# Kernel optimization log

Measured on AMD Instinct MI355X. Metric: run time of the kernel, lower is better.

The kernel has to match this reference:

```python
import jax, jax.numpy as jnp
import numpy as np

B, C, S, F = 128, 5, 512, 3
U = 256          # encoder units
RU = 2 * U       # decoder units / bidirectional encoder width


def _lstm_cell(x_t, h, c, Wk, Wr, b):
    # Keras LSTM gate order: i, f, g(cell), o
    z = x_t @ Wk + h @ Wr + b
    i, f, g, o = jnp.split(z, 4, axis=-1)
    c_new = jax.nn.sigmoid(f) * c + jax.nn.sigmoid(i) * jnp.tanh(g)
    h_new = jax.nn.sigmoid(o) * jnp.tanh(c_new)
    return h_new, c_new


def _masked_lstm(xs, mask, Wk, Wr, b, units):
    # xs: [B,S,D], mask: [B,S] bool. Keras semantics: masked steps carry
    # previous state and previous output (== previous h for LSTM).
    Bn = xs.shape[0]

    def step(carry, inp):
        h, c = carry
        x_t, m_t = inp
        h_n, c_n = _lstm_cell(x_t, h, c, Wk, Wr, b)
        m = m_t[:, None]
        h2 = jnp.where(m, h_n, h)
        c2 = jnp.where(m, c_n, c)
        return (h2, c2), h2

    init = (jnp.zeros((Bn, units), xs.dtype), jnp.zeros((Bn, units), xs.dtype))
    _, outs = jax.lax.scan(step, init, (jnp.swapaxes(xs, 0, 1), mask.T))
    return jnp.swapaxes(outs, 0, 1)  # [B,S,units]


def setup_inputs() -> dict:
    key = jax.random.key(0)
    k = jax.random.split(key, 10)
    s = 0.05
    rn = lambda kk, sh: jax.random.normal(kk, sh, jnp.float32) * s
    return {
        "x": jax.random.normal(k[0], (B, C, S, F), jnp.float32),
        "Wf_k": rn(k[1], (C, 4 * U)), "Wf_r": rn(k[2], (U, 4 * U)), "bf": jnp.zeros((4 * U,), jnp.float32),
        "Wb_k": rn(k[3], (C, 4 * U)), "Wb_r": rn(k[4], (U, 4 * U)), "bb": jnp.zeros((4 * U,), jnp.float32),
        "Wd_k": rn(k[5], (C, 4 * RU)), "Wd_r": rn(k[6], (RU, 4 * RU)), "bd": jnp.zeros((4 * RU,), jnp.float32),
        "W_attn": rn(k[7], (RU + C, 1)), "b_attn": jnp.zeros((1,), jnp.float32),
        "W_dense": rn(k[8], (RU + RU, C)), "b_dense": jnp.zeros((C,), jnp.float32),
    }


def reference(x, Wf_k, Wf_r, bf, Wb_k, Wb_r, bb, Wd_k, Wd_r, bd,
              W_attn, b_attn, W_dense, b_dense):
    xt = jnp.transpose(x, (0, 2, 1, 3))          # [B,S,C,F]
    mask = xt[:, :, 0, 2] != 0                   # tf.cast(..., bool)
    xs = xt[:, :, :, 0]                          # [B,S,C]

    fwd = _masked_lstm(xs, mask, Wf_k, Wf_r, bf, U)
    bwd = _masked_lstm(xs[:, ::-1], mask[:, ::-1], Wb_k, Wb_r, bb, U)[:, ::-1]
    enc = jnp.concatenate([fwd, bwd], axis=-1)   # [B,S,RU]

    # attention(concat([tile(x_t), enc])) is linear -> split the weight:
    Wx, We = W_attn[:C, 0], W_attn[C:, 0]
    enc_scores = jnp.einsum('bsd,d->bs', enc, We) + b_attn[0]  # [B,S]

    hidden0 = enc[:, -1, :]                      # [B,RU]
    x0 = xs[:, 0, :]                             # [B,C]

    def dec_step(carry, _):
        hidden, x_t = carry
        scores = enc_scores + (x_t @ Wx)[:, None]             # [B,S]
        alpha = jax.nn.softmax(scores, axis=1)
        attn = jnp.einsum('bs,bsd->bd', alpha, enc)           # [B,RU]
        # decoder LSTM on a single timestep, initial_state=[hidden, attn]
        h_new, _c = _lstm_cell(x_t, hidden, attn, Wd_k, Wd_r, bd)
        x_new = jnp.concatenate([h_new, attn], axis=-1) @ W_dense + b_dense
        return (h_new, x_new), x_new

    _, ys = jax.lax.scan(dec_step, (hidden0, x0), None, length=S - 1)  # [S-1,B,C]
    return jnp.transpose(ys, (1, 2, 0))[..., None]           # [B,C,S-1,1]
```

## Files before the change

kernel.cpp:

```cpp
#include <hip/hip_runtime.h>
#include <math.h>

#define BATCH 128
#define CCH 5
#define SEQ 512
#define UNITS 256
#define RU 512

#define ENC_N 33554432

__device__ __forceinline__ float sigmoidf_(float v) {
    return 1.0f / (1.0f + __expf(-v));
}
__device__ __forceinline__ float tanhf_(float v) {
    float e = __expf(2.0f * v);
    return 1.0f - 2.0f / (e + 1.0f);
}
__device__ __forceinline__ void astoref(float* p, float v) {
    __hip_atomic_store(p, v, __ATOMIC_RELAXED, __HIP_MEMORY_SCOPE_AGENT);
}
__device__ __forceinline__ void astorei(int* p, int v) {
    __hip_atomic_store(p, v, __ATOMIC_RELAXED, __HIP_MEMORY_SCOPE_AGENT);
}
__device__ __forceinline__ unsigned long long aloadu64(const unsigned long long* p) {
    return __hip_atomic_load(p, __ATOMIC_RELAXED, __HIP_MEMORY_SCOPE_AGENT);
}
__device__ __forceinline__ int aloadi(const int* p) {
    return __hip_atomic_load(p, __ATOMIC_RELAXED, __HIP_MEMORY_SCOPE_AGENT);
}

__global__ __attribute__((amdgpu_flat_work_group_size(1024, 1024),
                          amdgpu_waves_per_eu(4, 4)))
void encoder_kernel(const float* __restrict__ x,
                    const float* __restrict__ Wf_k, const float* __restrict__ Wf_r,
                    const float* __restrict__ bf,
                    const float* __restrict__ Wb_k, const float* __restrict__ Wb_r,
                    const float* __restrict__ bb,
                    float* __restrict__ enc, float* __restrict__ h_ex,
                    int* __restrict__ flags)
{
    const int bid  = blockIdx.x;
    const int dir  = bid >> 7;
    const int tile = (bid >> 3) & 15;
    const int jsl  = bid & 7;
    const int grp  = dir * 16 + tile;
    const int bg0  = tile * 8;
    const float* __restrict__ Wk   = dir ? Wb_k : Wf_k;
    const float* __restrict__ Wr   = dir ? Wb_r : Wf_r;
    const float* __restrict__ bias = dir ? bb : bf;
    const int tid = threadIdx.x;
    const int wv  = tid >> 6;
    const int l   = tid & 63;
    const int g0 = ((l >> 5) << 8) + jsl * 32 + (l & 31);

    __shared__ float zp[16][8][128];
    __shared__ float __align__(16) hLe[2][8][260];
    __shared__ float zred[8][128];
    __shared__ float WkL[5][128];
    __shared__ float biasL[128];
    __shared__ unsigned char mL[8][SEQ];
    __shared__ float xLe[8][8];

    for (int i = tid; i < 2 * 8 * 260; i += 1024) ((float*)hLe)[i] = 0.0f;
    if (tid < 128) biasL[tid] = bias[((tid >> 5) << 8) + jsl * 32 + (tid & 31)];
    if (tid >= 128 && tid < 768) {
        int i = tid - 128, c = i >> 7, cl = i & 127;
        WkL[c][cl] = Wk[c * 1024 + ((cl >> 5) << 8) + jsl * 32 + (cl & 31)];
    }
    for (int i = tid; i < 8 * SEQ; i += 1024) {
        int b = i >> 9, tt = i & (SEQ - 1);
        mL[b][tt] = (x[((size_t)((bg0 + b) * CCH) * SEQ + tt) * 3 + 2] != 0.0f) ? 1 : 0;
    }
    float wr0[16], wr1[16];
    {
        const float* wbase = Wr + (size_t)(wv * 16) * 1024 + g0;
        #pragma unroll
        for (int r = 0; r < 16; ++r) {
            wr0[r] = wbase[(size_t)r * 1024];
            wr1[r] = wbase[(size_t)r * 1024 + 512];
        }
        #pragma unroll
        for (int r = 0; r < 16; ++r)
            asm volatile("" : "+v"(wr0[r]), "+v"(wr1[r]));
    }
    float creg = 0.0f, hreg = 0.0f;
    __syncthreads();

    for (int t = 0; t < SEQ; ++t) {
        const int cur = t & 1;
        const int ts = dir ? (SEQ - 1 - t) : t;
        if (t > 0 && wv < 8) {
            if (l < 4) {
                const int* fp = &flags[(grp * 8 + wv) * 32 + l];
                int guard = 0;
                while (aloadi(fp) < t && guard < (1 << 26)) {
                    __builtin_amdgcn_s_sleep(1); ++guard;
                }
            }
            int b = l >> 3, u0 = wv * 32 + (l & 7) * 4;
            const unsigned long long* hsrc = (const unsigned long long*)
                &h_ex[(size_t)(dir * 2 + ((t - 1) & 1)) * 32768
                      + (size_t)(bg0 + b) * UNITS + u0];
            unsigned long long v0 = aloadu64(hsrc);
            unsigned long long v1 = aloadu64(hsrc + 1);
            float4 hv;
            ((unsigned long long*)&hv)[0] = v0;
            ((unsigned long long*)&hv)[1] = v1;
            *(float4*)&hLe[cur][b][u0] = hv;
        }
        if (tid >= 960 && tid < 1000) {
            int i = tid - 960, b = i / 5, c = i - b * 5;
            xLe[b][c] = x[((size_t)((bg0 + b) * CCH + c) * SEQ + ts) * 3];
        }
        __syncthreads();

        float accA[8], accB[8];
        #pragma unroll
        for (int b = 0; b < 8; ++b) {
            float a0 = 0.f, a1 = 0.f;
            const float4* hp = (const float4*)&hLe[cur][b][wv * 16];
            #pragma unroll
            for (int q = 0; q < 4; ++q) {
                float4 h4 = hp[q];
                a0 = fmaf(h4.x, wr0[4*q+0], a0); a1 = fmaf(h4.x, wr1[4*q+0], a1);
                a0 = fmaf(h4.y, wr0[4*q+1], a0); a1 = fmaf(h4.y, wr1[4*q+1], a1);
                a0 = fmaf(h4.z, wr0[4*q+2], a0); a1 = fmaf(h4.z, wr1[4*q+2], a1);
                a0 = fmaf(h4.w, wr0[4*q+3], a0); a1 = fmaf(h4.w, wr1[4*q+3], a1);
            }
            accA[b] = a0; accB[b] = a1;
        }
        #pragma unroll
        for (int b = 0; b < 8; ++b) {
            zp[wv][b][l]      = accA[b];
            zp[wv][b][64 + l] = accB[b];
        }
        __syncthreads();

        {
            int b = tid >> 7, cl = tid & 127;
            float sum = biasL[cl];
            #pragma unroll
            for (int s = 0; s < 16; ++s) sum += zp[s][b][cl];
            #pragma unroll
            for (int c = 0; c < 5; ++c) sum = fmaf(xLe[b][c], WkL[c][cl], sum);
            zred[b][cl] = sum;
        }
        __syncthreads();

        if (tid < 256) {
            int b = tid >> 5, u = tid & 31;
            float zi = zred[b][u];
            float zf = zred[b][32 + u];
            float zg = zred[b][64 + u];
            float zo = zred[b][96 + u];
            float cn = sigmoidf_(zf) * creg + sigmoidf_(zi) * tanhf_(zg);
            float hn = sigmoidf_(zo) * tanhf_(cn);
            int m = mL[b][ts];
            float h2 = m ? hn : hreg;
            float c2 = m ? cn : creg;
            creg = c2; hreg = h2;
            astoref(&h_ex[(size_t)(dir * 2 + cur) * 32768
                          + (size_t)(bg0 + b) * UNITS + jsl * 32 + u], h2);
            enc[((size_t)(bg0 + b) * SEQ + ts) * RU + dir * UNITS + jsl * 32 + u] = h2;
            asm volatile("s_waitcnt vmcnt(0)" ::: "memory");
            if (l == 0) astorei(&flags[(grp * 8 + jsl) * 32 + wv], t + 1);
        }
    }
}

__global__ __launch_bounds__(256)
void attn_kernel(const float* __restrict__ enc,
                 const float* __restrict__ W_attn, const float* __restrict__ b_attn,
                 const float* __restrict__ W_dense, const float* __restrict__ b_dense,
                 const float* __restrict__ x,
                 float* __restrict__ attn_ws, float* __restrict__ hidden_ws,
                 float* __restrict__ xbuf, float* __restrict__ xconst)
{
    const int b = blockIdx.x;
    const int tid = threadIdx.x;
    const int lane = tid & 63;
    const int wv = tid >> 6;

    __shared__ float WeL[RU];
    __shared__ float scoresL[SEQ];
    __shared__ float red[256];
    __shared__ float attnL[RU];

    WeL[tid]       = W_attn[CCH + tid];
    WeL[tid + 256] = W_attn[CCH + tid + 256];
    __syncthreads();

    const float* __restrict__ encb = enc + (size_t)b * SEQ * RU;
    const float batt = b_attn[0];

    for (int s = wv; s < SEQ; s += 4) {
        const float* row = encb + (size_t)s * RU;
        float p = 0.0f;
        #pragma unroll
        for (int i = 0; i < 8; ++i) {
            int d = lane * 8 + i;
            p = fmaf(row[d], WeL[d], p);
        }
        #pragma unroll
        for (int o = 32; o; o >>= 1) p += __shfl_xor(p, o);
        if (lane == 0) scoresL[s] = p + batt;
    }
    __syncthreads();

    float m = fmaxf(scoresL[tid], scoresL[tid + 256]);
    red[tid] = m;
    __syncthreads();
    for (int st = 128; st; st >>= 1) {
        if (tid < st) red[tid] = fmaxf(red[tid], red[tid + st]);
        __syncthreads();
    }
    const float mx = red[0];
    __syncthreads();
    float e0 = __expf(scoresL[tid] - mx);
    float e1 = __expf(scoresL[tid + 256] - mx);
    red[tid] = e0 + e1;
    __syncthreads();
    for (int st = 128; st; st >>= 1) {
        if (tid < st) red[tid] += red[tid + st];
        __syncthreads();
    }
    const float sinv = 1.0f / red[0];
    __syncthreads();
    scoresL[tid]       = e0 * sinv;
    scoresL[tid + 256] = e1 * sinv;
    __syncthreads();

    float a0 = 0.0f, a1 = 0.0f;
    for (int s = 0; s < SEQ; ++s) {
        float al = scoresL[s];
        a0 = fmaf(al, encb[(size_t)s * RU + tid], a0);
        a1 = fmaf(al, encb[(size_t)s * RU + tid + 256], a1);
    }
    attn_ws[(size_t)b * RU + tid]       = a0;
    attn_ws[(size_t)b * RU + tid + 256] = a1;
    attnL[tid] = a0;
    attnL[tid + 256] = a1;
    hidden_ws[(size_t)b * RU + tid]       = encb[(size_t)(SEQ - 1) * RU + tid];
    hidden_ws[(size_t)b * RU + tid + 256] = encb[(size_t)(SEQ - 1) * RU + tid + 256];
    if (tid < CCH) xbuf[b * CCH + tid] = x[((size_t)(b * CCH + tid) * SEQ + 0) * 3];
    __syncthreads();

    if (tid < CCH) {
        float acc = b_dense[tid];
        for (int d = 0; d < RU; ++d)
            acc = fmaf(attnL[d], W_dense[(RU + d) * CCH + tid], acc);
        xconst[b * CCH + tid] = acc;
    }
}

__global__ __attribute__((amdgpu_flat_work_group_size(1024, 1024),
                          amdgpu_waves_per_eu(4, 4)))
void decoder_kernel(const float* __restrict__ Wd_k, const float* __restrict__ Wd_r,
                    const float* __restrict__ bd,
                    const float* __restrict__ W_dense,
                    const float* __restrict__ attn_ws, const float* __restrict__ hidden_ws,
                    const float* __restrict__ xbuf, const float* __restrict__ xconst,
                    float* __restrict__ h_ex, int* __restrict__ flags,
                    float* __restrict__ out)
{
    const int bid  = blockIdx.x;
    const int tile = bid >> 4;
    const int jsl  = bid & 15;
    const int bg0  = tile * 8;
    const int tid  = threadIdx.x;
    const int wv   = tid >> 6;
    const int l    = tid & 63;
    const int g0 = ((l >> 5) << 9) + jsl * 32 + (l & 31);

    __shared__ float zp[16][8][128];
    __shared__ float __align__(16) hL[2][8][516];
    __shared__ float zred[8][128];
    __shared__ float WdL[RU * CCH];
    __shared__ float WkL[5][128];
    __shared__ float biasL[128];
    __shared__ float xL[8][8], xcL[8][8];

    for (int i = tid; i < RU * CCH; i += 1024) WdL[i] = W_dense[i];
    if (tid < 128) biasL[tid] = bd[((tid >> 5) << 9) + jsl * 32 + (tid & 31)];
    if (tid >= 128 && tid < 768) {
        int i = tid - 128, c = i >> 7, cl = i & 127;
        WkL[c][cl] = Wd_k[c * 2048 + ((cl >> 5) << 9) + jsl * 32 + (cl & 31)];
    }
    if (tid < 64) {
        int b = tid >> 3, c = tid & 7;
        if (c < 5) {
            xL[b][c]  = xbuf[(bg0 + b) * CCH + c];
            xcL[b][c] = xconst[(bg0 + b) * CCH + c];
        }
    }
    {
        int f = tid * 4, b = f >> 9, u = f & (RU - 1);
        *(float4*)&hL[0][b][u] = *(const float4*)&hidden_ws[(size_t)(bg0 + b) * RU + u];
    }
    float attR = 0.0f;
    if (tid < 256)
        attR = attn_ws[(size_t)(bg0 + (tid >> 5)) * RU + jsl * 32 + (tid & 31)];
    float wr0[32], wr1[32];
    {
        const float* wbase = Wd_r + (size_t)(wv * 32) * 2048 + g0;
        #pragma unroll
        for (int r = 0; r < 32; ++r) {
            wr0[r] = wbase[(size_t)r * 2048];
            wr1[r] = wbase[(size_t)r * 2048 + 1024];
        }
        #pragma unroll
        for (int r = 0; r < 32; ++r)
            asm volatile("" : "+v"(wr0[r]), "+v"(wr1[r]));
    }
    __syncthreads();

    for (int t = 0; t < SEQ - 1; ++t) {
        const int cur = t & 1;
        if (t > 0) {
            if (l < 4) {
                const int* fp = &flags[(tile * 16 + wv) * 32 + l];
                int guard = 0;
                while (aloadi(fp) < t && guard < (1 << 26)) {
                    __builtin_amdgcn_s_sleep(1); ++guard;
                }
            }
            int b = l >> 3, u0 = wv * 32 + (l & 7) * 4;
            const unsigned long long* hsrc = (const unsigned long long*)
                &h_ex[(size_t)((t - 1) & 1) * 65536 + (size_t)(bg0 + b) * RU + u0];
            unsigned long long v0 = aloadu64(hsrc);
            unsigned long long v1 = aloadu64(hsrc + 1);
            float4 hv;
            ((unsigned long long*)&hv)[0] = v0;
            ((unsigned long long*)&hv)[1] = v1;
            *(float4*)&hL[cur][b][u0] = hv;
        }
        __syncthreads();

        if (t > 0) {
            for (int it = wv; it < 40; it += 16) {
                int bb = it / 5, c = it - bb * 5;
                float p = 0.f;
                #pragma unroll
                for (int q = 0; q < 8; ++q) {
                    int uu = l + (q << 6);
                    p = fmaf(hL[cur][bb][uu], WdL[uu * CCH + c], p);
                }
                #pragma unroll
                for (int o = 32; o; o >>= 1) p += __shfl_xor(p, o);
                if (l == 0) xL[bb][c] = p + xcL[bb][c];
            }
        }

        float accA[8], accB[8];
        #pragma unroll
        for (int b = 0; b < 8; ++b) {
            float a0 = 0.f, a1 = 0.f;
            const float4* hp = (const float4*)&hL[cur][b][wv * 32];
            #pragma unroll
            for (int q = 0; q < 8; ++q) {
                float4 h4 = hp[q];
                a0 = fmaf(h4.x, wr0[4*q+0], a0); a1 = fmaf(h4.x, wr1[4*q+0], a1);
                a0 = fmaf(h4.y, wr0[4*q+1], a0); a1 = fmaf(h4.y, wr1[4*q+1], a1);
                a0 = fmaf(h4.z, wr0[4*q+2], a0); a1 = fmaf(h4.z, wr1[4*q+2], a1);
                a0 = fmaf(h4.w, wr0[4*q+3], a0); a1 = fmaf(h4.w, wr1[4*q+3], a1);
            }
            accA[b] = a0; accB[b] = a1;
        }
        #pragma unroll
        for (int b = 0; b < 8; ++b) {
            zp[wv][b][l]      = accA[b];
            zp[wv][b][64 + l] = accB[b];
        }
        __syncthreads();

        {
            int b = tid >> 7, cl = tid & 127;
            float sum = biasL[cl];
            #pragma unroll
            for (int s = 0; s < 16; ++s) sum += zp[s][b][cl];
            #pragma unroll
            for (int c = 0; c < 5; ++c) sum = fmaf(xL[b][c], WkL[c][cl], sum);
            zred[b][cl] = sum;
        }
        __syncthreads();

        if (tid < 256) {
            int b = tid >> 5, u = tid & 31;
            float zi = zred[b][u];
            float zf = zred[b][32 + u];
            float zg = zred[b][64 + u];
            float zo = zred[b][96 + u];
            float cn = sigmoidf_(zf) * attR + sigmoidf_(zi) * tanhf_(zg);
            float hn = sigmoidf_(zo) * tanhf_(cn);
            astoref(&h_ex[(size_t)cur * 65536
                          + (size_t)(bg0 + b) * RU + jsl * 32 + u], hn);
            asm volatile("s_waitcnt vmcnt(0)" ::: "memory");
            if (l == 0) astorei(&flags[(tile * 16 + jsl) * 32 + wv], t + 1);
        }
        if (t > 0 && jsl == 0 && tid >= 256 && tid < 296) {
            int i = tid - 256, bb = i / 5, c = i - bb * 5;
            out[(size_t)((bg0 + bb) * CCH + c) * (SEQ - 1) + (t - 1)] = xL[bb][c];
        }
    }

    if (jsl == 0) {
        const int t = SEQ - 1;
        const int cur = t & 1;
        if (l < 4) {
            const int* fp = &flags[(tile * 16 + wv) * 32 + l];
            int guard = 0;
            while (aloadi(fp) < t && guard < (1 << 26)) {
                __builtin_amdgcn_s_sleep(1); ++guard;
            }
        }
        int b = l >> 3, u0 = wv * 32 + (l & 7) * 4;
        const unsigned long long* hsrc = (const unsigned long long*)
            &h_ex[(size_t)((t - 1) & 1) * 65536 + (size_t)(bg0 + b) * RU + u0];
        unsigned long long v0 = aloadu64(hsrc);
        unsigned long long v1 = aloadu64(hsrc + 1);
        float4 hv;
        ((unsigned long long*)&hv)[0] = v0;
        ((unsigned long long*)&hv)[1] = v1;
        *(float4*)&hL[cur][b][u0] = hv;
        __syncthreads();
        for (int it = wv; it < 40; it += 16) {
            int bb = it / 5, c = it - bb * 5;
            float p = 0.f;
            #pragma unroll
            for (int q = 0; q < 8; ++q) {
                int uu = l + (q << 6);
                p = fmaf(hL[cur][bb][uu], WdL[uu * CCH + c], p);
            }
            #pragma unroll
            for (int o = 32; o; o >>= 1) p += __shfl_xor(p, o);
            if (l == 0)
                out[(size_t)((bg0 + bb) * CCH + c) * (SEQ - 1) + (t - 1)]
                    = p + xcL[bb][c];
        }
    }
}

extern "C" void kernel_launch(void* const* d_in, const int* in_sizes, int n_in,
                              void* d_out, int out_size, void* d_ws, size_t ws_size,
                              hipStream_t stream)
{
    const float* x       = (const float*)d_in[0];
    const float* Wf_k    = (const float*)d_in[1];
    const float* Wf_r    = (const float*)d_in[2];
    const float* bf      = (const float*)d_in[3];
    const float* Wb_k    = (const float*)d_in[4];
    const float* Wb_r    = (const float*)d_in[5];
    const float* bb      = (const float*)d_in[6];
    const float* Wd_k    = (const float*)d_in[7];
    const float* Wd_r    = (const float*)d_in[8];
    const float* bd      = (const float*)d_in[9];
    const float* W_attn  = (const float*)d_in[10];
    const float* b_attn  = (const float*)d_in[11];
    const float* W_dense = (const float*)d_in[12];
    const float* b_dense = (const float*)d_in[13];
    float* out = (float*)d_out;

    float* ws = (float*)d_ws;
    float* enc      = ws;
    float* attn_p   = ws + ENC_N;
    float* hidden_p = ws + ENC_N + 65536;
    float* xbuf_p   = ws + ENC_N + 131072;
    float* xconst_p = ws + ENC_N + 131712;
    float* h_ex_e   = ws + ENC_N;
    int*   flag_e   = (int*)(ws + ENC_N + 131072);
    int*   flag_d   = (int*)ws;
    float* h_ex_d   = ws + 8192;

    hipMemsetAsync(flag_e, 0, 8192 * sizeof(int), stream);
    encoder_kernel<<<256, 1024, 0, stream>>>(x, Wf_k, Wf_r, bf, Wb_k, Wb_r, bb,
                                             enc, h_ex_e, flag_e);
    attn_kernel<<<BATCH, 256, 0, stream>>>(enc, W_attn, b_attn, W_dense, b_dense, x,
                                           attn_p, hidden_p, xbuf_p, xconst_p);
    hipMemsetAsync(flag_d, 0, 8192 * sizeof(int), stream);
    decoder_kernel<<<256, 1024, 0, stream>>>(Wd_k, Wd_r, bd, W_dense,
                                             attn_p, hidden_p, xbuf_p, xconst_p,
                                             h_ex_d, flag_d, out);
}
```

Measured before the change: 5.736 ms.

## Replace flag-based inter-block sync with tagged 64-bit hidden-state exchange

Packs each hidden value with its timestep tag into one 64-bit atomic store, so consumers poll the data itself instead of separate flag arrays. This removes the store-wait-then-flag round trip and the extra flag polling latency on every recurrent step in both encoder and decoder. The encoder also double-buffers the input tile, which lets it drop one block barrier, and the decoder reorders its recurrent matvec ahead of the dense output step and folds the input projection into the gate stage. The cost is that the exchange buffers are twice as large and every wave now spins on the global loads, with only a bounded spin as a fallback.

```diff
diff --git a/kernel.cpp b/kernel.cpp
--- a/kernel.cpp
+++ b/kernel.cpp
@@ -16,17 +16,14 @@
     float e = __expf(2.0f * v);
     return 1.0f - 2.0f / (e + 1.0f);
 }
-__device__ __forceinline__ void astoref(float* p, float v) {
-    __hip_atomic_store(p, v, __ATOMIC_RELAXED, __HIP_MEMORY_SCOPE_AGENT);
-}
-__device__ __forceinline__ void astorei(int* p, int v) {
+__device__ __forceinline__ void astoreu64(unsigned long long* p, unsigned long long v) {
     __hip_atomic_store(p, v, __ATOMIC_RELAXED, __HIP_MEMORY_SCOPE_AGENT);
 }
 __device__ __forceinline__ unsigned long long aloadu64(const unsigned long long* p) {
     return __hip_atomic_load(p, __ATOMIC_RELAXED, __HIP_MEMORY_SCOPE_AGENT);
 }
-__device__ __forceinline__ int aloadi(const int* p) {
-    return __hip_atomic_load(p, __ATOMIC_RELAXED, __HIP_MEMORY_SCOPE_AGENT);
+__device__ __forceinline__ unsigned long long packht(unsigned tag, float h) {
+    return ((unsigned long long)tag << 32) | (unsigned long long)__float_as_uint(h);
 }
 
 __global__ __attribute__((amdgpu_flat_work_group_size(1024, 1024),
@@ -36,14 +33,12 @@
                     const float* __restrict__ bf,
                     const float* __restrict__ Wb_k, const float* __restrict__ Wb_r,
                     const float* __restrict__ bb,
-                    float* __restrict__ enc, float* __restrict__ h_ex,
-                    int* __restrict__ flags)
+                    float* __restrict__ enc, unsigned long long* __restrict__ hx)
 {
     const int bid  = blockIdx.x;
     const int dir  = bid >> 7;
     const int tile = (bid >> 3) & 15;
     const int jsl  = bid & 7;
-    const int grp  = dir * 16 + tile;
     const int bg0  = tile * 8;
     const float* __restrict__ Wk   = dir ? Wb_k : Wf_k;
     const float* __restrict__ Wr   = dir ? Wb_r : Wf_r;
@@ -59,7 +54,7 @@
     __shared__ float WkL[5][128];
     __shared__ float biasL[128];
     __shared__ unsigned char mL[8][SEQ];
-    __shared__ float xLe[8][8];
+    __shared__ float xLe[2][8][8];
 
     for (int i = tid; i < 2 * 8 * 260; i += 1024) ((float*)hLe)[i] = 0.0f;
     if (tid < 128) biasL[tid] = bias[((tid >> 5) << 8) + jsl * 32 + (tid & 31)];
@@ -89,39 +84,36 @@
     for (int t = 0; t < SEQ; ++t) {
         const int cur = t & 1;
         const int ts = dir ? (SEQ - 1 - t) : t;
-        if (t > 0 && wv < 8) {
-            if (l < 4) {
-                const int* fp = &flags[(grp * 8 + wv) * 32 + l];
-                int guard = 0;
-                while (aloadi(fp) < t && guard < (1 << 26)) {
-                    __builtin_amdgcn_s_sleep(1); ++guard;
-                }
-            }
-            int b = l >> 3, u0 = wv * 32 + (l & 7) * 4;
-            const unsigned long long* hsrc = (const unsigned long long*)
-                &h_ex[(size_t)(dir * 2 + ((t - 1) & 1)) * 32768
-                      + (size_t)(bg0 + b) * UNITS + u0];
-            unsigned long long v0 = aloadu64(hsrc);
-            unsigned long long v1 = aloadu64(hsrc + 1);
-            float4 hv;
-            ((unsigned long long*)&hv)[0] = v0;
-            ((unsigned long long*)&hv)[1] = v1;
-            *(float4*)&hLe[cur][b][u0] = hv;
+        if (t > 0) {
+            int b = l >> 3, u0 = wv * 16 + (l & 7) * 2;
+            const unsigned long long* hp = hx
+                + ((size_t)(dir * 2 + ((t - 1) & 1)) * 16 + tile) * 2048
+                + b * 256 + u0;
+            const unsigned tg = (unsigned)t;
+            unsigned long long v0, v1;
+            for (int it = 0;; ++it) {
+                v0 = aloadu64(hp);
+                v1 = aloadu64(hp + 1);
+                if ((unsigned)(v0 >> 32) == tg && (unsigned)(v1 >> 32) == tg) break;
+                if (it > (1 << 22)) break;
+                __builtin_amdgcn_s_sleep(1);
+            }
+            hLe[cur][b][u0]     = __uint_as_float((unsigned)v0);
+            hLe[cur][b][u0 + 1] = __uint_as_float((unsigned)v1);
         }
         if (tid >= 960 && tid < 1000) {
             int i = tid - 960, b = i / 5, c = i - b * 5;
-            xLe[b][c] = x[((size_t)((bg0 + b) * CCH + c) * SEQ + ts) * 3];
-        }
-        __syncthreads();
+            xLe[cur][b][c] = x[((size_t)((bg0 + b) * CCH + c) * SEQ + ts) * 3];
+        }
 
         float accA[8], accB[8];
         #pragma unroll
         for (int b = 0; b < 8; ++b) {
             float a0 = 0.f, a1 = 0.f;
-            const float4* hp = (const float4*)&hLe[cur][b][wv * 16];
+            const float4* hp4 = (const float4*)&hLe[cur][b][wv * 16];
             #pragma unroll
             for (int q = 0; q < 4; ++q) {
-                float4 h4 = hp[q];
+                float4 h4 = hp4[q];
                 a0 = fmaf(h4.x, wr0[4*q+0], a0); a1 = fmaf(h4.x, wr1[4*q+0], a1);
                 a0 = fmaf(h4.y, wr0[4*q+1], a0); a1 = fmaf(h4.y, wr1[4*q+1], a1);
                 a0 = fmaf(h4.z, wr0[4*q+2], a0); a1 = fmaf(h4.z, wr1[4*q+2], a1);
@@ -142,7 +134,7 @@
             #pragma unroll
             for (int s = 0; s < 16; ++s) sum += zp[s][b][cl];
             #pragma unroll
-            for (int c = 0; c < 5; ++c) sum = fmaf(xLe[b][c], WkL[c][cl], sum);
+            for (int c = 0; c < 5; ++c) sum = fmaf(xLe[cur][b][c], WkL[c][cl], sum);
             zred[b][cl] = sum;
         }
         __syncthreads();
@@ -159,11 +151,10 @@
             float h2 = m ? hn : hreg;
             float c2 = m ? cn : creg;
             creg = c2; hreg = h2;
-            astoref(&h_ex[(size_t)(dir * 2 + cur) * 32768
-                          + (size_t)(bg0 + b) * UNITS + jsl * 32 + u], h2);
+            astoreu64(&hx[((size_t)(dir * 2 + cur) * 16 + tile) * 2048
+                          + b * 256 + jsl * 32 + u],
+                      packht((unsigned)(t + 1), h2));
             enc[((size_t)(bg0 + b) * SEQ + ts) * RU + dir * UNITS + jsl * 32 + u] = h2;
-            asm volatile("s_waitcnt vmcnt(0)" ::: "memory");
-            if (l == 0) astorei(&flags[(grp * 8 + jsl) * 32 + wv], t + 1);
         }
     }
 }
@@ -260,7 +251,7 @@
                     const float* __restrict__ W_dense,
                     const float* __restrict__ attn_ws, const float* __restrict__ hidden_ws,
                     const float* __restrict__ xbuf, const float* __restrict__ xconst,
-                    float* __restrict__ h_ex, int* __restrict__ flags,
+                    unsigned long long* __restrict__ hx,
                     float* __restrict__ out)
 {
     const int bid  = blockIdx.x;
@@ -317,22 +308,46 @@
     for (int t = 0; t < SEQ - 1; ++t) {
         const int cur = t & 1;
         if (t > 0) {
-            if (l < 4) {
-                const int* fp = &flags[(tile * 16 + wv) * 32 + l];
-                int guard = 0;
-                while (aloadi(fp) < t && guard < (1 << 26)) {
-                    __builtin_amdgcn_s_sleep(1); ++guard;
-                }
-            }
             int b = l >> 3, u0 = wv * 32 + (l & 7) * 4;
-            const unsigned long long* hsrc = (const unsigned long long*)
-                &h_ex[(size_t)((t - 1) & 1) * 65536 + (size_t)(bg0 + b) * RU + u0];
-            unsigned long long v0 = aloadu64(hsrc);
-            unsigned long long v1 = aloadu64(hsrc + 1);
+            const unsigned long long* hp = hx
+                + ((size_t)((t - 1) & 1) * 16 + tile) * 4096 + b * 512 + u0;
+            const unsigned tg = (unsigned)t;
+            unsigned long long v0, v1, v2, v3;
+            for (int it = 0;; ++it) {
+                v0 = aloadu64(hp);     v1 = aloadu64(hp + 1);
+                v2 = aloadu64(hp + 2); v3 = aloadu64(hp + 3);
+                if ((unsigned)(v0 >> 32) == tg && (unsigned)(v1 >> 32) == tg &&
+                    (unsigned)(v2 >> 32) == tg && (unsigned)(v3 >> 32) == tg) break;
+                if (it > (1 << 22)) break;
+                __builtin_amdgcn_s_sleep(1);
+            }
             float4 hv;
-            ((unsigned long long*)&hv)[0] = v0;
-            ((unsigned long long*)&hv)[1] = v1;
+            hv.x = __uint_as_float((unsigned)v0);
+            hv.y = __uint_as_float((unsigned)v1);
+            hv.z = __uint_as_float((unsigned)v2);
+            hv.w = __uint_as_float((unsigned)v3);
             *(float4*)&hL[cur][b][u0] = hv;
+        }
+
+        float accA[8], accB[8];
+        #pragma unroll
+        for (int b = 0; b < 8; ++b) {
+            float a0 = 0.f, a1 = 0.f;
+            const float4* hp4 = (const float4*)&hL[cur][b][wv * 32];
+            #pragma unroll
+            for (int q = 0; q < 8; ++q) {
+                float4 h4 = hp4[q];
+                a0 = fmaf(h4.x, wr0[4*q+0], a0); a1 = fmaf(h4.x, wr1[4*q+0], a1);
+                a0 = fmaf(h4.y, wr0[4*q+1], a0); a1 = fmaf(h4.y, wr1[4*q+1], a1);
+                a0 = fmaf(h4.z, wr0[4*q+2], a0); a1 = fmaf(h4.z, wr1[4*q+2], a1);
+                a0 = fmaf(h4.w, wr0[4*q+3], a0); a1 = fmaf(h4.w, wr1[4*q+3], a1);
+            }
+            accA[b] = a0; accB[b] = a1;
+        }
+        #pragma unroll
+        for (int b = 0; b < 8; ++b) {
+            zp[wv][b][l]      = accA[b];
+            zp[wv][b][64 + l] = accB[b];
         }
         __syncthreads();
 
@@ -350,36 +365,11 @@
                 if (l == 0) xL[bb][c] = p + xcL[bb][c];
             }
         }
-
-        float accA[8], accB[8];
-        #pragma unroll
-        for (int b = 0; b < 8; ++b) {
-            float a0 = 0.f, a1 = 0.f;
-            const float4* hp = (const float4*)&hL[cur][b][wv * 32];
-            #pragma unroll
-            for (int q = 0; q < 8; ++q) {
-                float4 h4 = hp[q];
-                a0 = fmaf(h4.x, wr0[4*q+0], a0); a1 = fmaf(h4.x, wr1[4*q+0], a1);
-                a0 = fmaf(h4.y, wr0[4*q+1], a0); a1 = fmaf(h4.y, wr1[4*q+1], a1);
-                a0 = fmaf(h4.z, wr0[4*q+2], a0); a1 = fmaf(h4.z, wr1[4*q+2], a1);
-                a0 = fmaf(h4.w, wr0[4*q+3], a0); a1 = fmaf(h4.w, wr1[4*q+3], a1);
-            }
-            accA[b] = a0; accB[b] = a1;
-        }
-        #pragma unroll
-        for (int b = 0; b < 8; ++b) {
-            zp[wv][b][l]      = accA[b];
-            zp[wv][b][64 + l] = accB[b];
-        }
-        __syncthreads();
-
         {
             int b = tid >> 7, cl = tid & 127;
             float sum = biasL[cl];
             #pragma unroll
             for (int s = 0; s < 16; ++s) sum += zp[s][b][cl];
-            #pragma unroll
-            for (int c = 0; c < 5; ++c) sum = fmaf(xL[b][c], WkL[c][cl], sum);
             zred[b][cl] = sum;
         }
         __syncthreads();
@@ -390,12 +380,16 @@
             float zf = zred[b][32 + u];
             float zg = zred[b][64 + u];
             float zo = zred[b][96 + u];
+            #pragma unroll
+            for (int c = 0; c < 5; ++c) {
+                float xv = xL[b][c];
+                zi = fmaf(xv, WkL[c][u], zi);      zf = fmaf(xv, WkL[c][32 + u], zf);
+                zg = fmaf(xv, WkL[c][64 + u], zg); zo = fmaf(xv, WkL[c][96 + u], zo);
+            }
             float cn = sigmoidf_(zf) * attR + sigmoidf_(zi) * tanhf_(zg);
             float hn = sigmoidf_(zo) * tanhf_(cn);
-            astoref(&h_ex[(size_t)cur * 65536
-                          + (size_t)(bg0 + b) * RU + jsl * 32 + u], hn);
-            asm volatile("s_waitcnt vmcnt(0)" ::: "memory");
-            if (l == 0) astorei(&flags[(tile * 16 + jsl) * 32 + wv], t + 1);
+            astoreu64(&hx[((size_t)cur * 16 + tile) * 4096 + b * 512 + jsl * 32 + u],
+                      packht((unsigned)(t + 1), hn));
         }
         if (t > 0 && jsl == 0 && tid >= 256 && tid < 296) {
             int i = tid - 256, bb = i / 5, c = i - bb * 5;
@@ -406,21 +400,24 @@
     if (jsl == 0) {
         const int t = SEQ - 1;
         const int cur = t & 1;
-        if (l < 4) {
-            const int* fp = &flags[(tile * 16 + wv) * 32 + l];
-            int guard = 0;
-            while (aloadi(fp) < t && guard < (1 << 26)) {
-                __builtin_amdgcn_s_sleep(1); ++guard;
-            }
-        }
         int b = l >> 3, u0 = wv * 32 + (l & 7) * 4;
-        const unsigned long long* hsrc = (const unsigned long long*)
-            &h_ex[(size_t)((t - 1) & 1) * 65536 + (size_t)(bg0 + b) * RU + u0];
-        unsigned long long v0 = aloadu64(hsrc);
-        unsigned long long v1 = aloadu64(hsrc + 1);
+        const unsigned long long* hp = hx
+            + ((size_t)((t - 1) & 1) * 16 + tile) * 4096 + b * 512 + u0;
+        const unsigned tg = (unsigned)t;
+        unsigned long long v0, v1, v2, v3;
+        for (int it = 0;; ++it) {
+            v0 = aloadu64(hp);     v1 = aloadu64(hp + 1);
+            v2 = aloadu64(hp + 2); v3 = aloadu64(hp + 3);
+            if ((unsigned)(v0 >> 32) == tg && (unsigned)(v1 >> 32) == tg &&
+                (unsigned)(v2 >> 32) == tg && (unsigned)(v3 >> 32) == tg) break;
+            if (it > (1 << 22)) break;
+            __builtin_amdgcn_s_sleep(1);
+        }
         float4 hv;
-        ((unsigned long long*)&hv)[0] = v0;
-        ((unsigned long long*)&hv)[1] = v1;
+        hv.x = __uint_as_float((unsigned)v0);
+        hv.y = __uint_as_float((unsigned)v1);
+        hv.z = __uint_as_float((unsigned)v2);
+        hv.w = __uint_as_float((unsigned)v3);
         *(float4*)&hL[cur][b][u0] = hv;
         __syncthreads();
         for (int it = wv; it < 40; it += 16) {
@@ -466,18 +463,16 @@
     float* hidden_p = ws + ENC_N + 65536;
     float* xbuf_p   = ws + ENC_N + 131072;
     float* xconst_p = ws + ENC_N + 131712;
-    float* h_ex_e   = ws + ENC_N;
-    int*   flag_e   = (int*)(ws + ENC_N + 131072);
-    int*   flag_d   = (int*)ws;
-    float* h_ex_d   = ws + 8192;
-
-    hipMemsetAsync(flag_e, 0, 8192 * sizeof(int), stream);
+    unsigned long long* hx_e = (unsigned long long*)(ws + ENC_N);
+    unsigned long long* hx_d = (unsigned long long*)(ws + 8192);
+
+    hipMemsetAsync(hx_e, 0, 131072 * sizeof(unsigned long long), stream);
     encoder_kernel<<<256, 1024, 0, stream>>>(x, Wf_k, Wf_r, bf, Wb_k, Wb_r, bb,
-                                             enc, h_ex_e, flag_e);
+                                             enc, hx_e);
     attn_kernel<<<BATCH, 256, 0, stream>>>(enc, W_attn, b_attn, W_dense, b_dense, x,
                                            attn_p, hidden_p, xbuf_p, xconst_p);
-    hipMemsetAsync(flag_d, 0, 8192 * sizeof(int), stream);
+    hipMemsetAsync(hx_d, 0, 131072 * sizeof(unsigned long long), stream);
     decoder_kernel<<<256, 1024, 0, stream>>>(Wd_k, Wd_r, bd, W_dense,
                                              attn_p, hidden_p, xbuf_p, xconst_p,
-                                             h_ex_d, flag_d, out);
-}
+                                             hx_d, out);
+}
```

New measurement: 5.258 ms (median of 2 runs). 8.3% less time.
